# Optimization experiments

Hardware: AMD Instinct MI355X
Metric: run time of the kernel (lower is better)

## Reference

```python
import jax, jax.numpy as jnp
import numpy as np

B, T, H = 16, 2048, 1024

def setup_inputs() -> dict:
    key = jax.random.key(0)
    k1, k2, k3, k4 = jax.random.split(key, 4)
    stdv = 1.0 / np.sqrt(H)
    return {
        "hidden": jax.random.normal(k1, (B, H), dtype=jnp.float32),
        "encoder_outputs": jax.random.normal(k2, (B, T, 2 * H), dtype=jnp.float32),
        "W": jax.random.normal(k3, (H, 3 * H), dtype=jnp.float32) * stdv,  # nn.Linear(3H, H) weight
        "b": jnp.zeros((H,), dtype=jnp.float32),
        "v": jax.random.normal(k4, (H,), dtype=jnp.float32) * stdv,
    }

def reference(hidden, encoder_outputs, W, b, v):
    # hidden: (B,H); encoder_outputs: (B,T,2H)
    Bsz, Tlen, _ = encoder_outputs.shape
    Hrep = jnp.broadcast_to(hidden[:, None, :], (Bsz, Tlen, hidden.shape[-1]))  # (B,T,H)
    cat = jnp.concatenate([Hrep, encoder_outputs], axis=2)                      # (B,T,3H)
    energy = jnp.tanh(jnp.einsum('btk,hk->bth', cat, W) + b)                    # (B,T,H)
    scores = jnp.einsum('bth,h->bt', energy, v)[:, None, :]                     # (B,1,T), == bmm(v, energy^T)
    return jax.nn.softmax(scores, axis=2)
```

## Files before the change

kernel.cpp:

```cpp
#include <hip/hip_runtime.h>
#include <cstdint>

#define B_SZ 16
#define T_SZ 2048
#define H_SZ 1024
#define K_SZ 2048
#define M_SZ (B_SZ * T_SZ)

#define BM 128
#define BN 128
#define BK 64
#define LDK 72
#define KTILES (K_SZ / BK)

#define FBM 64
#define FBK 32
#define NSTEPS (K_SZ / FBK)

typedef _Float16 half8_t __attribute__((ext_vector_type(8)));
typedef _Float16 half4_t __attribute__((ext_vector_type(4)));
typedef float float4_t __attribute__((ext_vector_type(4)));

__device__ __forceinline__ void glds16(const _Float16* g, _Float16* l) {
    __builtin_amdgcn_global_load_lds(
        (const __attribute__((address_space(1))) void*)g,
        (__attribute__((address_space(3))) void*)l, 16, 0, 0);
}

__global__ __launch_bounds__(256) void cvt_w2_kernel(
    const float* __restrict__ W, _Float16* __restrict__ dst) {
    int idx8 = blockIdx.x * 256 + threadIdx.x;
    int n = idx8 >> 8, k = (idx8 & 255) * 8;
    const float* src = W + (size_t)n * 3072 + H_SZ + k;
    float4_t a = *(const float4_t*)(src);
    float4_t b = *(const float4_t*)(src + 4);
    half8_t h;
    h[0] = (_Float16)a[0]; h[1] = (_Float16)a[1];
    h[2] = (_Float16)a[2]; h[3] = (_Float16)a[3];
    h[4] = (_Float16)b[0]; h[5] = (_Float16)b[1];
    h[6] = (_Float16)b[2]; h[7] = (_Float16)b[3];
    int nblk = n >> 4, m16 = n & 15;
    int kblk = k >> 5, quad = (k >> 3) & 3;
    size_t di = (((size_t)nblk * 64 + kblk) * 64 + quad * 16 + m16) * 8;
    *(half8_t*)(dst + di) = h;
}

__global__ __launch_bounds__(256) void hpart_kernel(
    const float* __restrict__ hidden, const float* __restrict__ W,
    const float* __restrict__ bias, float* __restrict__ hpart) {
    int wave = (blockIdx.x * 256 + threadIdx.x) >> 6;
    int lane = threadIdx.x & 63;
    int b = wave >> 10;
    int h = wave & 1023;
    const float* wrow = W + (size_t)h * 3072;
    const float* hrow = hidden + b * H_SZ;
    int k0 = lane * 16;
    float acc = 0.f;
#pragma unroll
    for (int j = 0; j < 4; ++j) {
        float4_t wv = *(const float4_t*)(wrow + k0 + j * 4);
        float4_t hv = *(const float4_t*)(hrow + k0 + j * 4);
        acc += wv[0] * hv[0] + wv[1] * hv[1] + wv[2] * hv[2] + wv[3] * hv[3];
    }
#pragma unroll
    for (int off = 32; off >= 1; off >>= 1) acc += __shfl_xor(acc, off, 64);
    if (lane == 0) hpart[b * H_SZ + h] = acc + bias[h];
}

__global__ __launch_bounds__(512, 2) void fused2_attn_kernel(
    const float* __restrict__ enc, const _Float16* __restrict__ Bp,
    const float* __restrict__ hpart, const float* __restrict__ v,
    float* __restrict__ scores) {
    __shared__ __align__(16) _Float16 Als[2][FBM * FBK];
    __shared__ __align__(16) _Float16 Bls[2][64 * 512];

    const int tid = threadIdx.x;
    const int lane = tid & 63;
    const int w = tid >> 6;
    const int m16 = lane & 15, quad = lane >> 4;

    const int blockM = blockIdx.x;
    const int batch = blockM >> 5;

    const int arow = tid >> 3;
    const int ac8 = tid & 7;
    const float* Ap = enc + (size_t)(blockM * FBM + arow) * K_SZ + ac8 * 4;
    const int awbyte = arow * 64 +
        ((((ac8 >> 1) ^ ((arow >> 1) & 3)) << 4) | ((ac8 & 1) << 3));

    int afb[4];
#pragma unroll
    for (int tm = 0; tm < 4; ++tm) {
        int r = tm * 16 + m16;
        afb[tm] = r * 64 + ((quad ^ ((r >> 1) & 3)) << 4);
    }

    const _Float16* Bg = Bp + ((size_t)(w * 8) * 64) * 512 + lane * 8;

    float4_t acc[4][8];
#pragma unroll
    for (int i = 0; i < 4; ++i)
#pragma unroll
        for (int j = 0; j < 8; ++j) acc[i][j] = (float4_t){0.f, 0.f, 0.f, 0.f};

    {
        float4_t av = __builtin_nontemporal_load((const float4_t*)Ap);
#pragma unroll
        for (int i = 0; i < 8; ++i)
            glds16(Bg + (size_t)i * (64 * 512), &Bls[0][(w * 8 + i) * 512]);
        half4_t h;
        h[0] = (_Float16)av[0]; h[1] = (_Float16)av[1];
        h[2] = (_Float16)av[2]; h[3] = (_Float16)av[3];
        *(half4_t*)((char*)Als[0] + awbyte) = h;
    }
    __syncthreads();

    int cur = 0;
    for (int kt = 0; kt < NSTEPS; ++kt) {
        const bool pre = (kt + 1 < NSTEPS);
        float4_t av;
        if (pre) {
            av = __builtin_nontemporal_load(
                (const float4_t*)(Ap + (size_t)(kt + 1) * FBK));
#pragma unroll
            for (int i = 0; i < 8; ++i)
                glds16(Bg + (size_t)i * (64 * 512) + (size_t)(kt + 1) * 512,
                       &Bls[cur ^ 1][(w * 8 + i) * 512]);
        }
        half8_t af[4], bf[8];
#pragma unroll
        for (int tm = 0; tm < 4; ++tm)
            af[tm] = *(const half8_t*)((const char*)Als[cur] + afb[tm]);
#pragma unroll
        for (int tn = 0; tn < 8; ++tn)
            bf[tn] = *(const half8_t*)&Bls[cur][(w * 8 + tn) * 512 + lane * 8];

        __builtin_amdgcn_s_setprio(1);
#pragma unroll
        for (int tm = 0; tm < 4; ++tm)
#pragma unroll
            for (int tn = 0; tn < 8; ++tn)
                acc[tm][tn] = __builtin_amdgcn_mfma_f32_16x16x32_f16(
                    af[tm], bf[tn], acc[tm][tn], 0, 0, 0);
        __builtin_amdgcn_s_setprio(0);

        if (pre) {
            half4_t h;
            h[0] = (_Float16)av[0]; h[1] = (_Float16)av[1];
            h[2] = (_Float16)av[2]; h[3] = (_Float16)av[3];
            *(half4_t*)((char*)Als[cur ^ 1] + awbyte) = h;
        }
        __syncthreads();
        cur ^= 1;
    }

    float* sred = (float*)Als;

    float hpv[8], vv[8];
#pragma unroll
    for (int tn = 0; tn < 8; ++tn) {
        int col = w * 128 + tn * 16 + m16;
        hpv[tn] = hpart[batch * H_SZ + col];
        vv[tn] = v[col];
    }

#pragma unroll
    for (int tm = 0; tm < 4; ++tm) {
        float s0 = 0.f, s1 = 0.f, s2 = 0.f, s3 = 0.f;
#pragma unroll
        for (int tn = 0; tn < 8; ++tn) {
            s0 += tanhf(acc[tm][tn][0] + hpv[tn]) * vv[tn];
            s1 += tanhf(acc[tm][tn][1] + hpv[tn]) * vv[tn];
            s2 += tanhf(acc[tm][tn][2] + hpv[tn]) * vv[tn];
            s3 += tanhf(acc[tm][tn][3] + hpv[tn]) * vv[tn];
        }
#pragma unroll
        for (int off = 1; off < 16; off <<= 1) {
            s0 += __shfl_xor(s0, off, 64);
            s1 += __shfl_xor(s1, off, 64);
            s2 += __shfl_xor(s2, off, 64);
            s3 += __shfl_xor(s3, off, 64);
        }
        if (m16 == 0) {
            int rl = tm * 16 + quad * 4;
            sred[w * 64 + rl + 0] = s0;
            sred[w * 64 + rl + 1] = s1;
            sred[w * 64 + rl + 2] = s2;
            sred[w * 64 + rl + 3] = s3;
        }
    }
    __syncthreads();
    if (tid < FBM) {
        float t = 0.f;
#pragma unroll
        for (int i = 0; i < 8; ++i) t += sred[i * 64 + tid];
        scores[(size_t)blockM * FBM + tid] = t;
    }
}

__global__ __launch_bounds__(256) void softmax1_kernel(
    const float* __restrict__ scores, float* __restrict__ out) {
    __shared__ float red[256];
    const int b = blockIdx.x;
    const int tid = threadIdx.x;
    float sc[8];
    float mymax = -1e30f;
#pragma unroll
    for (int i = 0; i < 8; ++i) {
        float s = scores[b * T_SZ + i * 256 + tid];
        sc[i] = s;
        mymax = fmaxf(mymax, s);
    }
    red[tid] = mymax;
    __syncthreads();
    for (int off = 128; off >= 1; off >>= 1) {
        if (tid < off) red[tid] = fmaxf(red[tid], red[tid + off]);
        __syncthreads();
    }
    float mx = red[0];
    __syncthreads();
    float mysum = 0.f;
#pragma unroll
    for (int i = 0; i < 8; ++i) {
        sc[i] = expf(sc[i] - mx);
        mysum += sc[i];
    }
    red[tid] = mysum;
    __syncthreads();
    for (int off = 128; off >= 1; off >>= 1) {
        if (tid < off) red[tid] += red[tid + off];
        __syncthreads();
    }
    float inv = 1.0f / red[0];
#pragma unroll
    for (int i = 0; i < 8; ++i) out[b * T_SZ + i * 256 + tid] = sc[i] * inv;
}

__global__ __launch_bounds__(256, 2) void attn_gemm_kernel(
    const float* __restrict__ enc, const float* __restrict__ W,
    const float* __restrict__ hpart, const float* __restrict__ v,
    float* __restrict__ partial) {
    __shared__ _Float16 Afs[BM * LDK];
    __shared__ _Float16 Bfs[BN * LDK];
    __shared__ float hp_s[BN];
    __shared__ float v_s[BN];

    const int bidx = blockIdx.x;
    const int blockN = bidx & 7;
    const int blockM = bidx >> 3;
    const int tid = threadIdx.x;
    const int lane = tid & 63;
    const int w = tid >> 6;
    const int wm = w & 1, wn = w >> 1;
    const int m16 = lane & 15, quad = lane >> 4;

    const int n0 = blockN * BN;
    const int batch = blockM >> 4;

    if (tid < BN) {
        hp_s[tid] = hpart[batch * H_SZ + n0 + tid];
        v_s[tid] = v[n0 + tid];
    }

    float4_t acc[4][4];
#pragma unroll
    for (int i = 0; i < 4; ++i)
#pragma unroll
        for (int j = 0; j < 4; ++j) acc[i][j] = (float4_t){0.f, 0.f, 0.f, 0.f};

    const float* Abase = enc + (size_t)(blockM * BM) * K_SZ;
    const float* Bbase = W + (size_t)n0 * 3072 + H_SZ;

    for (int kt = 0; kt < KTILES; ++kt) {
        __syncthreads();
        const float* Asrc0 = Abase + kt * BK;
#pragma unroll
        for (int i = 0; i < 4; ++i) {
            int f8 = i * 256 + tid;
            int r = f8 >> 3, c8 = f8 & 7;
            const float* src = Asrc0 + (size_t)r * K_SZ + c8 * 8;
            float4_t lo = *(const float4_t*)(src);
            float4_t hi = *(const float4_t*)(src + 4);
            half8_t hv;
            hv[0] = (_Float16)lo[0]; hv[1] = (_Float16)lo[1];
            hv[2] = (_Float16)lo[2]; hv[3] = (_Float16)lo[3];
            hv[4] = (_Float16)hi[0]; hv[5] = (_Float16)hi[1];
            hv[6] = (_Float16)hi[2]; hv[7] = (_Float16)hi[3];
            *(half8_t*)&Afs[r * LDK + c8 * 8] = hv;
        }
        const float* Bsrc0 = Bbase + kt * BK;
#pragma unroll
        for (int i = 0; i < 4; ++i) {
            int f8 = i * 256 + tid;
            int r = f8 >> 3, c8 = f8 & 7;
            const float* src = Bsrc0 + (size_t)r * 3072 + c8 * 8;
            float4_t lo = *(const float4_t*)(src);
            float4_t hi = *(const float4_t*)(src + 4);
            half8_t hv;
            hv[0] = (_Float16)lo[0]; hv[1] = (_Float16)lo[1];
            hv[2] = (_Float16)lo[2]; hv[3] = (_Float16)lo[3];
            hv[4] = (_Float16)hi[0]; hv[5] = (_Float16)hi[1];
            hv[6] = (_Float16)hi[2]; hv[7] = (_Float16)hi[3];
            *(half8_t*)&Bfs[r * LDK + c8 * 8] = hv;
        }
        __syncthreads();
#pragma unroll
        for (int ks = 0; ks < 2; ++ks) {
            half8_t afrag[4], bfrag[4];
#pragma unroll
            for (int tm = 0; tm < 4; ++tm)
                afrag[tm] = *(const half8_t*)&Afs[(wm * 64 + tm * 16 + m16) * LDK + ks * 32 + quad * 8];
#pragma unroll
            for (int tn = 0; tn < 4; ++tn)
                bfrag[tn] = *(const half8_t*)&Bfs[(wn * 64 + tn * 16 + m16) * LDK + ks * 32 + quad * 8];
#pragma unroll
            for (int tm = 0; tm < 4; ++tm)
#pragma unroll
                for (int tn = 0; tn < 4; ++tn)
                    acc[tm][tn] = __builtin_amdgcn_mfma_f32_16x16x32_f16(
                        afrag[tm], bfrag[tn], acc[tm][tn], 0, 0, 0);
        }
    }

    const int slice = blockN * 2 + wn;
#pragma unroll
    for (int tm = 0; tm < 4; ++tm) {
        float s0 = 0.f, s1 = 0.f, s2 = 0.f, s3 = 0.f;
#pragma unroll
        for (int tn = 0; tn < 4; ++tn) {
            int nl = wn * 64 + tn * 16 + m16;
            float hpv = hp_s[nl];
            float vv = v_s[nl];
            s0 += tanhf(acc[tm][tn][0] + hpv) * vv;
            s1 += tanhf(acc[tm][tn][1] + hpv) * vv;
            s2 += tanhf(acc[tm][tn][2] + hpv) * vv;
            s3 += tanhf(acc[tm][tn][3] + hpv) * vv;
        }
#pragma unroll
        for (int off = 1; off < 16; off <<= 1) {
            s0 += __shfl_xor(s0, off, 64);
            s1 += __shfl_xor(s1, off, 64);
            s2 += __shfl_xor(s2, off, 64);
            s3 += __shfl_xor(s3, off, 64);
        }
        if (m16 == 0) {
            int gm = blockM * BM + wm * 64 + tm * 16 + quad * 4;
            float* dst = partial + (size_t)slice * M_SZ + gm;
            dst[0] = s0; dst[1] = s1; dst[2] = s2; dst[3] = s3;
        }
    }
}

__global__ __launch_bounds__(256) void softmax_kernel(
    const float* __restrict__ partial, float* __restrict__ out) {
    __shared__ float red[256];
    const int b = blockIdx.x;
    const int tid = threadIdx.x;
    float sc[8];
    float mymax = -1e30f;
#pragma unroll
    for (int i = 0; i < 8; ++i) {
        int t = i * 256 + tid;
        float s = 0.f;
#pragma unroll
        for (int sl = 0; sl < 16; ++sl) s += partial[(size_t)sl * M_SZ + b * T_SZ + t];
        sc[i] = s;
        mymax = fmaxf(mymax, s);
    }
    red[tid] = mymax;
    __syncthreads();
    for (int off = 128; off >= 1; off >>= 1) {
        if (tid < off) red[tid] = fmaxf(red[tid], red[tid + off]);
        __syncthreads();
    }
    float mx = red[0];
    __syncthreads();
    float mysum = 0.f;
#pragma unroll
    for (int i = 0; i < 8; ++i) {
        sc[i] = expf(sc[i] - mx);
        mysum += sc[i];
    }
    red[tid] = mysum;
    __syncthreads();
    for (int off = 128; off >= 1; off >>= 1) {
        if (tid < off) red[tid] += red[tid + off];
        __syncthreads();
    }
    float inv = 1.0f / red[0];
#pragma unroll
    for (int i = 0; i < 8; ++i) out[b * T_SZ + i * 256 + tid] = sc[i] * inv;
}

extern "C" void kernel_launch(void* const* d_in, const int* in_sizes, int n_in,
                              void* d_out, int out_size, void* d_ws, size_t ws_size,
                              hipStream_t stream) {
    const float* hidden = (const float*)d_in[0];
    const float* enc    = (const float*)d_in[1];
    const float* W      = (const float*)d_in[2];
    const float* bias   = (const float*)d_in[3];
    const float* v      = (const float*)d_in[4];
    float* out = (float*)d_out;

    float* hpart  = (float*)d_ws;
    float* scores = hpart + B_SZ * H_SZ;
    _Float16* w2h = (_Float16*)(scores + M_SZ);
    const size_t need = (size_t)((char*)(w2h + (size_t)H_SZ * K_SZ) - (char*)d_ws);

    hipLaunchKernelGGL(hpart_kernel, dim3(4096), dim3(256), 0, stream,
                       hidden, W, bias, hpart);
    if (ws_size >= need) {
        hipLaunchKernelGGL(cvt_w2_kernel, dim3(1024), dim3(256), 0, stream, W, w2h);
        hipLaunchKernelGGL(fused2_attn_kernel, dim3(M_SZ / FBM), dim3(512), 0, stream,
                           enc, w2h, hpart, v, scores);
        hipLaunchKernelGGL(softmax1_kernel, dim3(B_SZ), dim3(256), 0, stream,
                           scores, out);
    } else {
        float* partial = scores;
        hipLaunchKernelGGL(attn_gemm_kernel, dim3(2048), dim3(256), 0, stream,
                           enc, W, hpart, v, partial);
        hipLaunchKernelGGL(softmax_kernel, dim3(B_SZ), dim3(256), 0, stream,
                           partial, out);
    }
}
```

Baseline: 572.2 us.

## Split fused attention GEMM over N slices with B fragments loaded from global

Replaces the 64x1024-output-per-block fused kernel with a 64x256 tile per block, launching four N-slice blocks per M tile. Each slice writes a partial score and the softmax kernel sums the partials. The B operand now goes straight from global/L2 into registers with a software prefetch instead of being staged in LDS via global_load_lds, and BK doubles to 64. This cuts LDS use and raises occupancy (256 threads, 3 blocks per CU). The cost is reading and converting each encoder row four times, once per N slice.

```diff
diff --git a/kernel.cpp b/kernel.cpp
--- a/kernel.cpp
+++ b/kernel.cpp
@@ -13,19 +13,15 @@
 #define LDK 72
 #define KTILES (K_SZ / BK)
 
-#define FBM 64
-#define FBK 32
-#define NSTEPS (K_SZ / FBK)
+#define XBM 64
+#define XBN 256
+#define XBK 64
+#define XSTEPS (K_SZ / XBK)
+#define XSLICES 4
 
 typedef _Float16 half8_t __attribute__((ext_vector_type(8)));
 typedef _Float16 half4_t __attribute__((ext_vector_type(4)));
 typedef float float4_t __attribute__((ext_vector_type(4)));
-
-__device__ __forceinline__ void glds16(const _Float16* g, _Float16* l) {
-    __builtin_amdgcn_global_load_lds(
-        (const __attribute__((address_space(1))) void*)g,
-        (__attribute__((address_space(3))) void*)l, 16, 0, 0);
-}
 
 __global__ __launch_bounds__(256) void cvt_w2_kernel(
     const float* __restrict__ W, _Float16* __restrict__ dst) {
@@ -67,88 +63,131 @@
     if (lane == 0) hpart[b * H_SZ + h] = acc + bias[h];
 }
 
-__global__ __launch_bounds__(512, 2) void fused2_attn_kernel(
+__global__ __launch_bounds__(256, 3) void fused3_attn_kernel(
     const float* __restrict__ enc, const _Float16* __restrict__ Bp,
     const float* __restrict__ hpart, const float* __restrict__ v,
-    float* __restrict__ scores) {
-    __shared__ __align__(16) _Float16 Als[2][FBM * FBK];
-    __shared__ __align__(16) _Float16 Bls[2][64 * 512];
+    float* __restrict__ partial) {
+    __shared__ __align__(16) _Float16 Als[2][XBM * XBK];
 
     const int tid = threadIdx.x;
     const int lane = tid & 63;
     const int w = tid >> 6;
     const int m16 = lane & 15, quad = lane >> 4;
 
-    const int blockM = blockIdx.x;
+    const int bid = blockIdx.x;
+    const int blockN = bid & 3;
+    const int blockM = bid >> 2;
     const int batch = blockM >> 5;
-
-    const int arow = tid >> 3;
-    const int ac8 = tid & 7;
-    const float* Ap = enc + (size_t)(blockM * FBM + arow) * K_SZ + ac8 * 4;
-    const int awbyte = arow * 64 +
-        ((((ac8 >> 1) ^ ((arow >> 1) & 3)) << 4) | ((ac8 & 1) << 3));
-
-    int afb[4];
-#pragma unroll
-    for (int tm = 0; tm < 4; ++tm) {
-        int r = tm * 16 + m16;
-        afb[tm] = r * 64 + ((quad ^ ((r >> 1) & 3)) << 4);
-    }
-
-    const _Float16* Bg = Bp + ((size_t)(w * 8) * 64) * 512 + lane * 8;
-
-    float4_t acc[4][8];
+    const int row0 = blockM * XBM;
+
+    const int ar = tid >> 2, ag2 = tid & 3;
+    const float* Ap = enc + (size_t)(row0 + ar) * K_SZ + ag2 * 16;
+    const int k8 = ar & 7;
+    const int wb0 = ar * 128 + (((ag2 * 2) ^ k8) << 4);
+    const int wb1 = ar * 128 + (((ag2 * 2 + 1) ^ k8) << 4);
+
+    int afb[2][4];
+#pragma unroll
+    for (int ks = 0; ks < 2; ++ks)
+#pragma unroll
+        for (int tm = 0; tm < 4; ++tm) {
+            int r = tm * 16 + m16;
+            afb[ks][tm] = r * 128 + (((ks * 4 + quad) ^ (r & 7)) << 4);
+        }
+
+    const _Float16* Bg[4];
+#pragma unroll
+    for (int tn = 0; tn < 4; ++tn)
+        Bg[tn] = Bp + ((size_t)((blockN * 16 + w * 4 + tn) * 64) * 64 + lane) * 8;
+
+    float4_t acc[4][4];
 #pragma unroll
     for (int i = 0; i < 4; ++i)
 #pragma unroll
-        for (int j = 0; j < 8; ++j) acc[i][j] = (float4_t){0.f, 0.f, 0.f, 0.f};
+        for (int j = 0; j < 4; ++j) acc[i][j] = (float4_t){0.f, 0.f, 0.f, 0.f};
 
     {
-        float4_t av = __builtin_nontemporal_load((const float4_t*)Ap);
-#pragma unroll
-        for (int i = 0; i < 8; ++i)
-            glds16(Bg + (size_t)i * (64 * 512), &Bls[0][(w * 8 + i) * 512]);
-        half4_t h;
-        h[0] = (_Float16)av[0]; h[1] = (_Float16)av[1];
-        h[2] = (_Float16)av[2]; h[3] = (_Float16)av[3];
-        *(half4_t*)((char*)Als[0] + awbyte) = h;
-    }
+        float4_t a0 = __builtin_nontemporal_load((const float4_t*)Ap);
+        float4_t a1 = __builtin_nontemporal_load((const float4_t*)(Ap + 4));
+        float4_t a2 = __builtin_nontemporal_load((const float4_t*)(Ap + 8));
+        float4_t a3 = __builtin_nontemporal_load((const float4_t*)(Ap + 12));
+        half8_t h0, h1;
+        h0[0] = (_Float16)a0[0]; h0[1] = (_Float16)a0[1];
+        h0[2] = (_Float16)a0[2]; h0[3] = (_Float16)a0[3];
+        h0[4] = (_Float16)a1[0]; h0[5] = (_Float16)a1[1];
+        h0[6] = (_Float16)a1[2]; h0[7] = (_Float16)a1[3];
+        h1[0] = (_Float16)a2[0]; h1[1] = (_Float16)a2[1];
+        h1[2] = (_Float16)a2[2]; h1[3] = (_Float16)a2[3];
+        h1[4] = (_Float16)a3[0]; h1[5] = (_Float16)a3[1];
+        h1[6] = (_Float16)a3[2]; h1[7] = (_Float16)a3[3];
+        *(half8_t*)((char*)Als[0] + wb0) = h0;
+        *(half8_t*)((char*)Als[0] + wb1) = h1;
+    }
+    half8_t bfA[4];
+#pragma unroll
+    for (int tn = 0; tn < 4; ++tn) bfA[tn] = *(const half8_t*)(Bg[tn]);
     __syncthreads();
 
     int cur = 0;
-    for (int kt = 0; kt < NSTEPS; ++kt) {
-        const bool pre = (kt + 1 < NSTEPS);
-        float4_t av;
+    for (int kt = 0; kt < XSTEPS; ++kt) {
+        const bool pre = (kt + 1 < XSTEPS);
+        half8_t bfB[4];
+#pragma unroll
+        for (int tn = 0; tn < 4; ++tn)
+            bfB[tn] = *(const half8_t*)(Bg[tn] + (size_t)(kt * 2 + 1) * 512);
+        float4_t a0, a1, a2, a3;
         if (pre) {
-            av = __builtin_nontemporal_load(
-                (const float4_t*)(Ap + (size_t)(kt + 1) * FBK));
-#pragma unroll
-            for (int i = 0; i < 8; ++i)
-                glds16(Bg + (size_t)i * (64 * 512) + (size_t)(kt + 1) * 512,
-                       &Bls[cur ^ 1][(w * 8 + i) * 512]);
-        }
-        half8_t af[4], bf[8];
-#pragma unroll
-        for (int tm = 0; tm < 4; ++tm)
-            af[tm] = *(const half8_t*)((const char*)Als[cur] + afb[tm]);
-#pragma unroll
-        for (int tn = 0; tn < 8; ++tn)
-            bf[tn] = *(const half8_t*)&Bls[cur][(w * 8 + tn) * 512 + lane * 8];
-
-        __builtin_amdgcn_s_setprio(1);
-#pragma unroll
-        for (int tm = 0; tm < 4; ++tm)
-#pragma unroll
-            for (int tn = 0; tn < 8; ++tn)
-                acc[tm][tn] = __builtin_amdgcn_mfma_f32_16x16x32_f16(
-                    af[tm], bf[tn], acc[tm][tn], 0, 0, 0);
-        __builtin_amdgcn_s_setprio(0);
-
+            const float* Apn = Ap + (size_t)(kt + 1) * XBK;
+            a0 = __builtin_nontemporal_load((const float4_t*)Apn);
+            a1 = __builtin_nontemporal_load((const float4_t*)(Apn + 4));
+            a2 = __builtin_nontemporal_load((const float4_t*)(Apn + 8));
+            a3 = __builtin_nontemporal_load((const float4_t*)(Apn + 12));
+        }
+        {
+            half8_t af[4];
+#pragma unroll
+            for (int tm = 0; tm < 4; ++tm)
+                af[tm] = *(const half8_t*)((const char*)Als[cur] + afb[0][tm]);
+            __builtin_amdgcn_s_setprio(1);
+#pragma unroll
+            for (int tm = 0; tm < 4; ++tm)
+#pragma unroll
+                for (int tn = 0; tn < 4; ++tn)
+                    acc[tm][tn] = __builtin_amdgcn_mfma_f32_16x16x32_f16(
+                        af[tm], bfA[tn], acc[tm][tn], 0, 0, 0);
+            __builtin_amdgcn_s_setprio(0);
+        }
         if (pre) {
-            half4_t h;
-            h[0] = (_Float16)av[0]; h[1] = (_Float16)av[1];
-            h[2] = (_Float16)av[2]; h[3] = (_Float16)av[3];
-            *(half4_t*)((char*)Als[cur ^ 1] + awbyte) = h;
+#pragma unroll
+            for (int tn = 0; tn < 4; ++tn)
+                bfA[tn] = *(const half8_t*)(Bg[tn] + (size_t)(kt * 2 + 2) * 512);
+        }
+        {
+            half8_t af[4];
+#pragma unroll
+            for (int tm = 0; tm < 4; ++tm)
+                af[tm] = *(const half8_t*)((const char*)Als[cur] + afb[1][tm]);
+            __builtin_amdgcn_s_setprio(1);
+#pragma unroll
+            for (int tm = 0; tm < 4; ++tm)
+#pragma unroll
+                for (int tn = 0; tn < 4; ++tn)
+                    acc[tm][tn] = __builtin_amdgcn_mfma_f32_16x16x32_f16(
+                        af[tm], bfB[tn], acc[tm][tn], 0, 0, 0);
+            __builtin_amdgcn_s_setprio(0);
+        }
+        if (pre) {
+            half8_t h0, h1;
+            h0[0] = (_Float16)a0[0]; h0[1] = (_Float16)a0[1];
+            h0[2] = (_Float16)a0[2]; h0[3] = (_Float16)a0[3];
+            h0[4] = (_Float16)a1[0]; h0[5] = (_Float16)a1[1];
+            h0[6] = (_Float16)a1[2]; h0[7] = (_Float16)a1[3];
+            h1[0] = (_Float16)a2[0]; h1[1] = (_Float16)a2[1];
+            h1[2] = (_Float16)a2[2]; h1[3] = (_Float16)a2[3];
+            h1[4] = (_Float16)a3[0]; h1[5] = (_Float16)a3[1];
+            h1[6] = (_Float16)a3[2]; h1[7] = (_Float16)a3[3];
+            *(half8_t*)((char*)Als[cur ^ 1] + wb0) = h0;
+            *(half8_t*)((char*)Als[cur ^ 1] + wb1) = h1;
         }
         __syncthreads();
         cur ^= 1;
@@ -156,19 +195,19 @@
 
     float* sred = (float*)Als;
 
-    float hpv[8], vv[8];
-#pragma unroll
-    for (int tn = 0; tn < 8; ++tn) {
-        int col = w * 128 + tn * 16 + m16;
-        hpv[tn] = hpart[batch * H_SZ + col];
-        vv[tn] = v[col];
+    float hpv[4], vv[4];
+#pragma unroll
+    for (int tn = 0; tn < 4; ++tn) {
+        int gcol = blockN * XBN + w * 64 + tn * 16 + m16;
+        hpv[tn] = hpart[batch * H_SZ + gcol];
+        vv[tn] = v[gcol];
     }
 
 #pragma unroll
     for (int tm = 0; tm < 4; ++tm) {
         float s0 = 0.f, s1 = 0.f, s2 = 0.f, s3 = 0.f;
 #pragma unroll
-        for (int tn = 0; tn < 8; ++tn) {
+        for (int tn = 0; tn < 4; ++tn) {
             s0 += tanhf(acc[tm][tn][0] + hpv[tn]) * vv[tn];
             s1 += tanhf(acc[tm][tn][1] + hpv[tn]) * vv[tn];
             s2 += tanhf(acc[tm][tn][2] + hpv[tn]) * vv[tn];
@@ -190,16 +229,16 @@
         }
     }
     __syncthreads();
-    if (tid < FBM) {
+    if (tid < XBM) {
         float t = 0.f;
 #pragma unroll
-        for (int i = 0; i < 8; ++i) t += sred[i * 64 + tid];
-        scores[(size_t)blockM * FBM + tid] = t;
-    }
-}
-
-__global__ __launch_bounds__(256) void softmax1_kernel(
-    const float* __restrict__ scores, float* __restrict__ out) {
+        for (int i = 0; i < 4; ++i) t += sred[i * 64 + tid];
+        partial[(size_t)blockN * M_SZ + row0 + tid] = t;
+    }
+}
+
+__global__ __launch_bounds__(256) void softmax4_kernel(
+    const float* __restrict__ partial, float* __restrict__ out) {
     __shared__ float red[256];
     const int b = blockIdx.x;
     const int tid = threadIdx.x;
@@ -207,7 +246,11 @@
     float mymax = -1e30f;
 #pragma unroll
     for (int i = 0; i < 8; ++i) {
-        float s = scores[b * T_SZ + i * 256 + tid];
+        int t = i * 256 + tid;
+        float s = 0.f;
+#pragma unroll
+        for (int sl = 0; sl < XSLICES; ++sl)
+            s += partial[(size_t)sl * M_SZ + b * T_SZ + t];
         sc[i] = s;
         mymax = fmaxf(mymax, s);
     }
@@ -402,21 +445,20 @@
     const float* v      = (const float*)d_in[4];
     float* out = (float*)d_out;
 
-    float* hpart  = (float*)d_ws;
-    float* scores = hpart + B_SZ * H_SZ;
-    _Float16* w2h = (_Float16*)(scores + M_SZ);
+    float* hpart   = (float*)d_ws;
+    float* partial = hpart + B_SZ * H_SZ;
+    _Float16* w2h  = (_Float16*)(partial + XSLICES * M_SZ);
     const size_t need = (size_t)((char*)(w2h + (size_t)H_SZ * K_SZ) - (char*)d_ws);
 
     hipLaunchKernelGGL(hpart_kernel, dim3(4096), dim3(256), 0, stream,
                        hidden, W, bias, hpart);
     if (ws_size >= need) {
         hipLaunchKernelGGL(cvt_w2_kernel, dim3(1024), dim3(256), 0, stream, W, w2h);
-        hipLaunchKernelGGL(fused2_attn_kernel, dim3(M_SZ / FBM), dim3(512), 0, stream,
-                           enc, w2h, hpart, v, scores);
-        hipLaunchKernelGGL(softmax1_kernel, dim3(B_SZ), dim3(256), 0, stream,
-                           scores, out);
+        hipLaunchKernelGGL(fused3_attn_kernel, dim3((M_SZ / XBM) * XSLICES),
+                           dim3(256), 0, stream, enc, w2h, hpart, v, partial);
+        hipLaunchKernelGGL(softmax4_kernel, dim3(B_SZ), dim3(256), 0, stream,
+                           partial, out);
     } else {
-        float* partial = scores;
         hipLaunchKernelGGL(attn_gemm_kernel, dim3(2048), dim3(256), 0, stream,
                            enc, W, hpart, v, partial);
         hipLaunchKernelGGL(softmax_kernel, dim3(B_SZ), dim3(256), 0, stream,
```

After: 681.3 us. 19.1% more time.
